# Kernel optimization log

Measured on AMD Instinct MI355X. Metric: run time of the kernel, lower is better.

Reference implementation:

```python
import jax, jax.numpy as jnp
import numpy as np

B, S, QD = 4, 2048, 1024
NH, KVH, DH = 16, 4, 64
WIN = 256  # sliding_window


def setup_inputs() -> dict:
    key = jax.random.key(0)
    ks = jax.random.split(key, 5)
    s = QD ** -0.5
    return {
        "hidden_states": jax.random.normal(ks[0], (B, S, QD), jnp.float32),
        "Wq": jax.random.normal(ks[1], (QD, NH * DH), jnp.float32) * s,
        "Wk": jax.random.normal(ks[2], (QD, KVH * DH), jnp.float32) * s,
        "Wv": jax.random.normal(ks[3], (QD, KVH * DH), jnp.float32) * s,
        "Wo": jax.random.normal(ks[4], (NH * DH, QD), jnp.float32) * s,
    }


def reference(hidden_states, Wq, Wk, Wv, Wo):
    x = hidden_states
    # QKV projections (torch Linear, no bias)
    q = (x @ Wq).reshape(B, S, NH, DH).transpose(0, 2, 1, 3)    # [B,NH,S,DH]
    k = (x @ Wk).reshape(B, S, KVH, DH).transpose(0, 2, 1, 3)   # [B,KVH,S,DH]
    v = (x @ Wv).reshape(B, S, KVH, DH).transpose(0, 2, 1, 3)
    # GQA: instead of repeat_interleave on k/v, group query heads per kv head
    g = NH // KVH
    qg = q.reshape(B, KVH, g, S, DH)
    scale = DH ** -0.5
    scores = jnp.einsum('bkgsd,bktd->bkgst', qg, k) * scale      # [B,KVH,g,S,S]
    # Sliding-window mask: torch SDPA treats a FLOAT mask as ADDITIVE, and the
    # original builds a 0/1 float mask (1 where |i-j| <= window). Faithful: add it.
    idx = jnp.arange(S)
    win = (jnp.abs(idx[:, None] - idx[None, :]) <= WIN).astype(scores.dtype)  # [S,S]
    scores = scores + win  # broadcast over B,KVH,g (same mask for all batch/heads)
    attn = jax.nn.softmax(scores, axis=-1)
    out = jnp.einsum('bkgst,bktd->bkgsd', attn, v)               # [B,KVH,g,S,DH]
    out = out.reshape(B, NH, S, DH).transpose(0, 2, 1, 3).reshape(B, S, NH * DH)
    return out @ Wo
```

## Files before the change

### kernel.cpp

```cpp
#include <hip/hip_runtime.h>
#include <hip/hip_bf16.h>


using short8 = __attribute__((ext_vector_type(8))) short;
using f32x4  = __attribute__((ext_vector_type(4))) float;
using f32x16 = __attribute__((ext_vector_type(16))) float;
using uint2v = __attribute__((ext_vector_type(2))) unsigned int;

#define GLDS(g, l) __builtin_amdgcn_global_load_lds( \
    (const __attribute__((address_space(1))) void*)(g), \
    (__attribute__((address_space(3))) void*)(l), 16, 0, 0)

__device__ __forceinline__ unsigned short f2bf(float f) {
  union { float f; unsigned u; } v; v.f = f;
  unsigned r = v.u + 0x7fffu + ((v.u >> 16) & 1u);
  return (unsigned short)(r >> 16);
}

__device__ __forceinline__ unsigned cvtpk(float lo, float hi) {
  unsigned r;
  asm("v_cvt_pk_bf16_f32 %0, %1, %2" : "=v"(r) : "v"(lo), "v"(hi));
  return r;
}

__global__ void cvt_x_kernel(const float* __restrict__ X, unsigned short* __restrict__ Xb) {
  int i = (blockIdx.x * blockDim.x + threadIdx.x) * 4;
  float4 v = *reinterpret_cast<const float4*>(X + i);
  ushort4 o;
  o.x = f2bf(v.x); o.y = f2bf(v.y); o.z = f2bf(v.z); o.w = f2bf(v.w);
  *reinterpret_cast<ushort4*>(Xb + i) = o;
}

__global__ __launch_bounds__(256) void wtr_kernel(
    const float* __restrict__ Wq, const float* __restrict__ Wk,
    const float* __restrict__ Wv, const float* __restrict__ Wo,
    unsigned short* __restrict__ WqkvT, unsigned short* __restrict__ WoT)
{
  __shared__ float tile[32][33];
  const int bx = blockIdx.x;
  const int by = blockIdx.y;
  const float* src; unsigned short* dst; int C, ct;
  if (by < 32)      { src = Wq; dst = WqkvT;               C = 1024; ct = by; }
  else if (by < 40) { src = Wk; dst = WqkvT + 1024 * 1024; C = 256;  ct = by - 32; }
  else if (by < 48) { src = Wv; dst = WqkvT + 1280 * 1024; C = 256;  ct = by - 40; }
  else              { src = Wo; dst = WoT;                 C = 1024; ct = by - 48; }
  const int tx = threadIdx.x & 31, ty = threadIdx.x >> 5;
  const int c0 = ct * 32, r0 = bx * 32;
#pragma unroll
  for (int i = 0; i < 4; ++i)
    tile[ty + i * 8][tx] = src[(size_t)(r0 + ty + i * 8) * C + c0 + tx];
  __syncthreads();
#pragma unroll
  for (int i = 0; i < 4; ++i) {
    int c = ty + i * 8;
    dst[(size_t)(c0 + c) * 1024 + r0 + tx] = f2bf(tile[tx][c]);
  }
}

template<int MODE>
__global__ __launch_bounds__(256) void gemm_bt_kernel(
    const unsigned short* __restrict__ A, const unsigned short* __restrict__ Bt,
    unsigned short* __restrict__ Qo, unsigned short* __restrict__ Ko,
    unsigned short* __restrict__ Vto, float* __restrict__ Co)
{
  __shared__ __align__(16) unsigned short As[128 * 32];
  __shared__ __align__(16) unsigned short Bs[128 * 32];
  const int m0 = blockIdx.x * 128;
  const int n0 = (MODE == 2 ? 1280 : 0) + blockIdx.y * 128;
  const int t = threadIdx.x;
  const int w = t >> 6, l = t & 63;
  const int wr = w >> 1, wc = w & 1;

  f32x4 acc[4][4] = {};

  const size_t aoff = (size_t)(m0 + w * 16 + (l >> 2)) * 1024 + (size_t)((l & 3) * 8);
  const size_t boff = (size_t)(n0 + w * 16 + (l >> 2)) * 1024 + (size_t)((l & 3) * 8);

  for (int kt = 0; kt < 1024; kt += 32) {
    GLDS(A  + aoff + kt,             &As[w * 512]);
    GLDS(A  + aoff + 64 * 1024 + kt, &As[(w + 4) * 512]);
    GLDS(Bt + boff + kt,             &Bs[w * 512]);
    GLDS(Bt + boff + 64 * 1024 + kt, &Bs[(w + 4) * 512]);
    __syncthreads();

    short8 af[4], bfr[4];
#pragma unroll
    for (int mi = 0; mi < 4; ++mi) {
      int row = wr * 64 + mi * 16 + (l & 15);
      af[mi] = *reinterpret_cast<const short8*>(&As[row * 32 + (l >> 4) * 8]);
    }
#pragma unroll
    for (int ni = 0; ni < 4; ++ni) {
      int row = wc * 64 + ni * 16 + (l & 15);
      bfr[ni] = *reinterpret_cast<const short8*>(&Bs[row * 32 + (l >> 4) * 8]);
    }
#pragma unroll
    for (int mi = 0; mi < 4; ++mi)
#pragma unroll
      for (int ni = 0; ni < 4; ++ni) {
        if (MODE == 0)
          acc[mi][ni] = __builtin_amdgcn_mfma_f32_16x16x32_bf16(bfr[ni], af[mi], acc[mi][ni], 0, 0, 0);
        else
          acc[mi][ni] = __builtin_amdgcn_mfma_f32_16x16x32_bf16(af[mi], bfr[ni], acc[mi][ni], 0, 0, 0);
      }
    __syncthreads();
  }

  const int lo = (l >> 4) * 4;

  if (MODE == 0) {
#pragma unroll
    for (int mi = 0; mi < 4; ++mi) {
      const int tok = m0 + wr * 64 + mi * 16 + (l & 15);
      const int bb = tok >> 11, ss = tok & 2047;
      const size_t bT = (size_t)bb * 16, T5 = ss >> 5, q5 = ss & 31;
#pragma unroll
      for (int ni = 0; ni < 4; ++ni) {
        const int ddb = n0 + wc * 64 + ni * 16;
        uint2 wv;
        wv.x = cvtpk(acc[mi][ni][0], acc[mi][ni][1]);
        wv.y = cvtpk(acc[mi][ni][2], acc[mi][ni][3]);
        size_t base; unsigned short* dstp;
        if (ddb < 1024) {
          int hh = ddb >> 6, kk = (ddb >> 4) & 3;
          base = ((((size_t)(bb * 16 + hh)) * 64 + T5) * 4 + kk) * 512; dstp = Qo;
        } else {
          int kvh = (ddb - 1024) >> 6, kk = (ddb >> 4) & 3;
          base = ((((size_t)(bb * 4 + kvh)) * 64 + T5) * 4 + kk) * 512; dstp = Ko;
        }
        *reinterpret_cast<uint2*>(dstp + base + (lo >> 3) * 256 + q5 * 8 + (lo & 7)) = wv;
      }
    }
  } else if (MODE == 2) {
#pragma unroll
    for (int ni = 0; ni < 4; ++ni) {
      const int dd = n0 + wc * 64 + ni * 16 + (l & 15);
      const int kvh = (dd - 1280) >> 6, d6 = dd & 63;
#pragma unroll
      for (int mi = 0; mi < 4; ++mi) {
        const int tokb = m0 + wr * 64 + mi * 16 + lo;
        const int bb = tokb >> 11, ss = tokb & 2047;
        const int T5 = ss >> 5;
        const int f = (d6 >> 5) * 2 + (mi & 1);
        uint2 wv;
        wv.x = cvtpk(acc[mi][ni][0], acc[mi][ni][1]);
        wv.y = cvtpk(acc[mi][ni][2], acc[mi][ni][3]);
        size_t base = ((((size_t)(bb * 4 + kvh)) * 64 + T5) * 4 + f) * 512;
        *reinterpret_cast<uint2*>(Vto + base + ((lo >> 3) & 1) * 256 + (d6 & 31) * 8 + (lo & 7)) = wv;
      }
    }
  } else {
#pragma unroll
    for (int mi = 0; mi < 4; ++mi)
#pragma unroll
      for (int ni = 0; ni < 4; ++ni)
#pragma unroll
        for (int r = 0; r < 4; ++r) {
          int m = m0 + wr * 64 + mi * 16 + lo + r;
          int n = n0 + wc * 64 + ni * 16 + (l & 15);
          Co[((size_t)m << 10) + n] = acc[mi][ni][r];
        }
  }
}

__global__ __launch_bounds__(256, 4) void attn_kernel(
    const unsigned short* __restrict__ Qf, const unsigned short* __restrict__ Kf,
    const unsigned short* __restrict__ Vf, unsigned short* __restrict__ AO)
{
  const int t = threadIdx.x, w = t >> 6, l = t & 63;
  const int hi = l >> 5, ln = l & 31;

  const int orig = blockIdx.x;
  const int swz = (orig & 7) * 128 + (orig >> 3);
  const int hf = swz >> 4;
  const int qt = swz & 15;
  const int b = hf >> 4, h = hf & 15, kvh = h >> 2;
  const int q0 = qt * 128 + w * 32;
  const int qrow = q0 + ln;

  const unsigned short* Qp = Qf + (((size_t)hf * 64 + qt * 4 + w) * 4) * 512;
  const unsigned short* Kt = Kf + ((size_t)(b * 4 + kvh) * 256) * 512 + l * 8;
  const unsigned short* Vt = Vf + ((size_t)(b * 4 + kvh) * 256) * 512 + l * 8;

  short8 qf[4];
#pragma unroll
  for (int kk = 0; kk < 4; ++kk)
    qf[kk] = *reinterpret_cast<const short8*>(Qp + kk * 512 + l * 8);

  f32x16 oA = {}, oB = {};
  float lsum = 0.f;
  const float C1  = 0.125f * 1.44269504f;
  const float L2E = 1.44269504f;
  const float FM  = 12.0f;

  for (int T = 0; T < 64; ++T) {
    short8 kf0 = *reinterpret_cast<const short8*>(Kt);
    short8 kf1 = *reinterpret_cast<const short8*>(Kt + 512);
    short8 kf2 = *reinterpret_cast<const short8*>(Kt + 1024);
    short8 kf3 = *reinterpret_cast<const short8*>(Kt + 1536);
    f32x16 s = {};
    s = __builtin_amdgcn_mfma_f32_32x32x16_bf16(kf0, qf[0], s, 0, 0, 0);
    s = __builtin_amdgcn_mfma_f32_32x32x16_bf16(kf1, qf[1], s, 0, 0, 0);
    s = __builtin_amdgcn_mfma_f32_32x32x16_bf16(kf2, qf[2], s, 0, 0, 0);
    s = __builtin_amdgcn_mfma_f32_32x32x16_bf16(kf3, qf[3], s, 0, 0, 0);
    short8 vf0 = *reinterpret_cast<const short8*>(Vt);
    short8 vf1 = *reinterpret_cast<const short8*>(Vt + 512);
    short8 vf2 = *reinterpret_cast<const short8*>(Vt + 1024);
    short8 vf3 = *reinterpret_cast<const short8*>(Vt + 1536);
    Kt += 2048; Vt += 2048;

    const int kv0 = T * 32;
    const int d = q0 - kv0;
    float p[16];
    if (d == 256 || d == -256) {
      const int qmb = qrow - kv0 - 4 * hi;
#pragma unroll
      for (int r = 0; r < 16; ++r) {
        const int kc = (r & 3) + 8 * (r >> 2);
        int df = qmb - kc; df = df < 0 ? -df : df;
        p[r] = __builtin_amdgcn_exp2f(
            __builtin_fmaf(s[r], C1, (df <= 256 ? L2E : 0.f) - FM));
      }
    } else {
      const float cc = ((d <= 224 && d >= -224) ? L2E : 0.f) - FM;
#pragma unroll
      for (int i = 0; i < 16; ++i)
        p[i] = __builtin_amdgcn_exp2f(__builtin_fmaf(s[i], C1, cc));
    }

    float s8[8], s4[4];
#pragma unroll
    for (int i = 0; i < 8; ++i) s8[i] = p[i] + p[i + 8];
#pragma unroll
    for (int i = 0; i < 4; ++i) s4[i] = s8[i] + s8[i + 4];
    float sum = (s4[0] + s4[1]) + (s4[2] + s4[3]);
    {
      uint2v sw = __builtin_amdgcn_permlane32_swap(__float_as_uint(sum), __float_as_uint(sum), false, false);
      sum = __uint_as_float(sw[0]) + __uint_as_float(sw[1]);
    }
    lsum += sum;

#pragma unroll
    for (int ks = 0; ks < 2; ++ks) {
      unsigned a0 = cvtpk(p[ks * 8 + 0], p[ks * 8 + 1]);
      unsigned a1 = cvtpk(p[ks * 8 + 2], p[ks * 8 + 3]);
      unsigned b0 = cvtpk(p[ks * 8 + 4], p[ks * 8 + 5]);
      unsigned b1 = cvtpk(p[ks * 8 + 6], p[ks * 8 + 7]);
      uint2v s0 = __builtin_amdgcn_permlane32_swap(a0, b0, false, false);
      uint2v s1 = __builtin_amdgcn_permlane32_swap(a1, b1, false, false);
      union { unsigned u[4]; short8 v; } pf;
      pf.u[0] = s0[0]; pf.u[1] = s1[0]; pf.u[2] = s0[1]; pf.u[3] = s1[1];
      oA = __builtin_amdgcn_mfma_f32_32x32x16_bf16(ks ? vf1 : vf0, pf.v, oA, 0, 0, 0);
      oB = __builtin_amdgcn_mfma_f32_32x32x16_bf16(ks ? vf3 : vf2, pf.v, oB, 0, 0, 0);
    }
  }

  const float inv = 1.f / lsum;
  unsigned short* Op = AO + ((size_t)(b * 2048 + qrow)) * 1024 + h * 64;
#pragma unroll
  for (int qd = 0; qd < 4; ++qd) {
    uint2 wv;
    wv.x = cvtpk(oA[4 * qd + 0] * inv, oA[4 * qd + 1] * inv);
    wv.y = cvtpk(oA[4 * qd + 2] * inv, oA[4 * qd + 3] * inv);
    *reinterpret_cast<uint2*>(Op + qd * 8 + hi * 4) = wv;
  }
#pragma unroll
  for (int qd = 0; qd < 4; ++qd) {
    uint2 wv;
    wv.x = cvtpk(oB[4 * qd + 0] * inv, oB[4 * qd + 1] * inv);
    wv.y = cvtpk(oB[4 * qd + 2] * inv, oB[4 * qd + 3] * inv);
    *reinterpret_cast<uint2*>(Op + 32 + qd * 8 + hi * 4) = wv;
  }
}

extern "C" void kernel_launch(void* const* d_in, const int* in_sizes, int n_in,
                              void* d_out, int out_size, void* d_ws, size_t ws_size,
                              hipStream_t stream)
{
  const float* X  = (const float*)d_in[0];
  const float* Wq = (const float*)d_in[1];
  const float* Wk = (const float*)d_in[2];
  const float* Wv = (const float*)d_in[3];
  const float* Wo = (const float*)d_in[4];
  float* out = (float*)d_out;
  char* ws = (char*)d_ws;

  unsigned short* Xb    = (unsigned short*)(ws);
  unsigned short* WqkvT = (unsigned short*)(ws + 16777216);
  unsigned short* WoT   = (unsigned short*)(ws + 19922944);
  unsigned short* Q     = (unsigned short*)(ws + 22020096);
  unsigned short* Kc    = (unsigned short*)(ws + 38797312);
  unsigned short* Vt    = (unsigned short*)(ws + 42991616);
  unsigned short* AO    = (unsigned short*)(ws + 47185920);

  cvt_x_kernel<<<8192, 256, 0, stream>>>(X, Xb);
  wtr_kernel<<<dim3(32, 80), 256, 0, stream>>>(Wq, Wk, Wv, Wo, WqkvT, WoT);

  gemm_bt_kernel<0><<<dim3(64, 10), 256, 0, stream>>>(Xb, WqkvT, Q, Kc, nullptr, nullptr);
  gemm_bt_kernel<2><<<dim3(64, 2),  256, 0, stream>>>(Xb, WqkvT, nullptr, nullptr, Vt, nullptr);
  attn_kernel<<<1024, 256, 0, stream>>>(Q, Kc, Vt, AO);
  gemm_bt_kernel<1><<<dim3(64, 8),  256, 0, stream>>>(AO, WoT, nullptr, nullptr, nullptr, out);
}
```

Before: 200.8 us.

## Fuse fp32-to-bf16 conversion of X into QKV GEMM and merge Q/K/V launches

Drops the standalone kernel that converts X to bf16. The QKV GEMM now reads fp32 X directly, converts it in registers with v_cvt_pk_bf16_f32, and writes the bf16 tile to LDS. The separate QK and V GEMM launches are merged into one 64x12 grid that chooses operand order and epilogue from n0. This removes a full bf16 round trip of X through memory and one launch. In exchange, each QKV block re-reads fp32 X, twice the bytes of bf16, across 12 column tiles, and loses the async global_load_lds path for the A operand.

```diff
diff --git a/kernel.cpp b/kernel.cpp
--- a/kernel.cpp
+++ b/kernel.cpp
@@ -21,14 +21,6 @@
   unsigned r;
   asm("v_cvt_pk_bf16_f32 %0, %1, %2" : "=v"(r) : "v"(lo), "v"(hi));
   return r;
-}
-
-__global__ void cvt_x_kernel(const float* __restrict__ X, unsigned short* __restrict__ Xb) {
-  int i = (blockIdx.x * blockDim.x + threadIdx.x) * 4;
-  float4 v = *reinterpret_cast<const float4*>(X + i);
-  ushort4 o;
-  o.x = f2bf(v.x); o.y = f2bf(v.y); o.z = f2bf(v.z); o.w = f2bf(v.w);
-  *reinterpret_cast<ushort4*>(Xb + i) = o;
 }
 
 __global__ __launch_bounds__(256) void wtr_kernel(
@@ -57,16 +49,15 @@
   }
 }
 
-template<int MODE>
-__global__ __launch_bounds__(256) void gemm_bt_kernel(
-    const unsigned short* __restrict__ A, const unsigned short* __restrict__ Bt,
+__global__ __launch_bounds__(256) void qkv_gemm_kernel(
+    const float* __restrict__ X, const unsigned short* __restrict__ Bt,
     unsigned short* __restrict__ Qo, unsigned short* __restrict__ Ko,
-    unsigned short* __restrict__ Vto, float* __restrict__ Co)
+    unsigned short* __restrict__ Vto)
 {
   __shared__ __align__(16) unsigned short As[128 * 32];
   __shared__ __align__(16) unsigned short Bs[128 * 32];
   const int m0 = blockIdx.x * 128;
-  const int n0 = (MODE == 2 ? 1280 : 0) + blockIdx.y * 128;
+  const int n0 = blockIdx.y * 128;
   const int t = threadIdx.x;
   const int w = t >> 6, l = t & 63;
   const int wr = w >> 1, wc = w & 1;
@@ -75,12 +66,24 @@
 
   const size_t aoff = (size_t)(m0 + w * 16 + (l >> 2)) * 1024 + (size_t)((l & 3) * 8);
   const size_t boff = (size_t)(n0 + w * 16 + (l >> 2)) * 1024 + (size_t)((l & 3) * 8);
+  unsigned short* Aw0 = &As[w * 512 + l * 8];
+  unsigned short* Aw1 = &As[(w + 4) * 512 + l * 8];
+  const bool qk = (n0 < 1280);
 
   for (int kt = 0; kt < 1024; kt += 32) {
-    GLDS(A  + aoff + kt,             &As[w * 512]);
-    GLDS(A  + aoff + 64 * 1024 + kt, &As[(w + 4) * 512]);
     GLDS(Bt + boff + kt,             &Bs[w * 512]);
     GLDS(Bt + boff + 64 * 1024 + kt, &Bs[(w + 4) * 512]);
+    float4 fa0 = *reinterpret_cast<const float4*>(X + aoff + kt);
+    float4 fa1 = *reinterpret_cast<const float4*>(X + aoff + kt + 4);
+    float4 fb0 = *reinterpret_cast<const float4*>(X + aoff + 64 * 1024 + kt);
+    float4 fb1 = *reinterpret_cast<const float4*>(X + aoff + 64 * 1024 + kt + 4);
+    uint4 ua, ub;
+    ua.x = cvtpk(fa0.x, fa0.y); ua.y = cvtpk(fa0.z, fa0.w);
+    ua.z = cvtpk(fa1.x, fa1.y); ua.w = cvtpk(fa1.z, fa1.w);
+    ub.x = cvtpk(fb0.x, fb0.y); ub.y = cvtpk(fb0.z, fb0.w);
+    ub.z = cvtpk(fb1.x, fb1.y); ub.w = cvtpk(fb1.z, fb1.w);
+    *reinterpret_cast<uint4*>(Aw0) = ua;
+    *reinterpret_cast<uint4*>(Aw1) = ub;
     __syncthreads();
 
     short8 af[4], bfr[4];
@@ -94,26 +97,30 @@
       int row = wc * 64 + ni * 16 + (l & 15);
       bfr[ni] = *reinterpret_cast<const short8*>(&Bs[row * 32 + (l >> 4) * 8]);
     }
-#pragma unroll
-    for (int mi = 0; mi < 4; ++mi)
-#pragma unroll
-      for (int ni = 0; ni < 4; ++ni) {
-        if (MODE == 0)
+    if (qk) {
+#pragma unroll
+      for (int mi = 0; mi < 4; ++mi)
+#pragma unroll
+        for (int ni = 0; ni < 4; ++ni)
           acc[mi][ni] = __builtin_amdgcn_mfma_f32_16x16x32_bf16(bfr[ni], af[mi], acc[mi][ni], 0, 0, 0);
-        else
+    } else {
+#pragma unroll
+      for (int mi = 0; mi < 4; ++mi)
+#pragma unroll
+        for (int ni = 0; ni < 4; ++ni)
           acc[mi][ni] = __builtin_amdgcn_mfma_f32_16x16x32_bf16(af[mi], bfr[ni], acc[mi][ni], 0, 0, 0);
-      }
+    }
     __syncthreads();
   }
 
   const int lo = (l >> 4) * 4;
 
-  if (MODE == 0) {
+  if (qk) {
 #pragma unroll
     for (int mi = 0; mi < 4; ++mi) {
       const int tok = m0 + wr * 64 + mi * 16 + (l & 15);
       const int bb = tok >> 11, ss = tok & 2047;
-      const size_t bT = (size_t)bb * 16, T5 = ss >> 5, q5 = ss & 31;
+      const int T5 = ss >> 5, q5 = ss & 31;
 #pragma unroll
       for (int ni = 0; ni < 4; ++ni) {
         const int ddb = n0 + wc * 64 + ni * 16;
@@ -131,7 +138,7 @@
         *reinterpret_cast<uint2*>(dstp + base + (lo >> 3) * 256 + q5 * 8 + (lo & 7)) = wv;
       }
     }
-  } else if (MODE == 2) {
+  } else {
 #pragma unroll
     for (int ni = 0; ni < 4; ++ni) {
       const int dd = n0 + wc * 64 + ni * 16 + (l & 15);
@@ -149,18 +156,62 @@
         *reinterpret_cast<uint2*>(Vto + base + ((lo >> 3) & 1) * 256 + (d6 & 31) * 8 + (lo & 7)) = wv;
       }
     }
-  } else {
+  }
+}
+
+__global__ __launch_bounds__(256) void outproj_gemm_kernel(
+    const unsigned short* __restrict__ A, const unsigned short* __restrict__ Bt,
+    float* __restrict__ Co)
+{
+  __shared__ __align__(16) unsigned short As[128 * 32];
+  __shared__ __align__(16) unsigned short Bs[128 * 32];
+  const int m0 = blockIdx.x * 128;
+  const int n0 = blockIdx.y * 128;
+  const int t = threadIdx.x;
+  const int w = t >> 6, l = t & 63;
+  const int wr = w >> 1, wc = w & 1;
+
+  f32x4 acc[4][4] = {};
+
+  const size_t aoff = (size_t)(m0 + w * 16 + (l >> 2)) * 1024 + (size_t)((l & 3) * 8);
+  const size_t boff = (size_t)(n0 + w * 16 + (l >> 2)) * 1024 + (size_t)((l & 3) * 8);
+
+  for (int kt = 0; kt < 1024; kt += 32) {
+    GLDS(A  + aoff + kt,             &As[w * 512]);
+    GLDS(A  + aoff + 64 * 1024 + kt, &As[(w + 4) * 512]);
+    GLDS(Bt + boff + kt,             &Bs[w * 512]);
+    GLDS(Bt + boff + 64 * 1024 + kt, &Bs[(w + 4) * 512]);
+    __syncthreads();
+
+    short8 af[4], bfr[4];
+#pragma unroll
+    for (int mi = 0; mi < 4; ++mi) {
+      int row = wr * 64 + mi * 16 + (l & 15);
+      af[mi] = *reinterpret_cast<const short8*>(&As[row * 32 + (l >> 4) * 8]);
+    }
+#pragma unroll
+    for (int ni = 0; ni < 4; ++ni) {
+      int row = wc * 64 + ni * 16 + (l & 15);
+      bfr[ni] = *reinterpret_cast<const short8*>(&Bs[row * 32 + (l >> 4) * 8]);
+    }
 #pragma unroll
     for (int mi = 0; mi < 4; ++mi)
 #pragma unroll
       for (int ni = 0; ni < 4; ++ni)
-#pragma unroll
-        for (int r = 0; r < 4; ++r) {
-          int m = m0 + wr * 64 + mi * 16 + lo + r;
-          int n = n0 + wc * 64 + ni * 16 + (l & 15);
-          Co[((size_t)m << 10) + n] = acc[mi][ni][r];
-        }
-  }
+        acc[mi][ni] = __builtin_amdgcn_mfma_f32_16x16x32_bf16(af[mi], bfr[ni], acc[mi][ni], 0, 0, 0);
+    __syncthreads();
+  }
+
+#pragma unroll
+  for (int mi = 0; mi < 4; ++mi)
+#pragma unroll
+    for (int ni = 0; ni < 4; ++ni)
+#pragma unroll
+      for (int r = 0; r < 4; ++r) {
+        int m = m0 + wr * 64 + mi * 16 + (l >> 4) * 4 + r;
+        int n = n0 + wc * 64 + ni * 16 + (l & 15);
+        Co[((size_t)m << 10) + n] = acc[mi][ni][r];
+      }
 }
 
 __global__ __launch_bounds__(256, 4) void attn_kernel(
@@ -285,19 +336,15 @@
   float* out = (float*)d_out;
   char* ws = (char*)d_ws;
 
-  unsigned short* Xb    = (unsigned short*)(ws);
-  unsigned short* WqkvT = (unsigned short*)(ws + 16777216);
-  unsigned short* WoT   = (unsigned short*)(ws + 19922944);
-  unsigned short* Q     = (unsigned short*)(ws + 22020096);
-  unsigned short* Kc    = (unsigned short*)(ws + 38797312);
-  unsigned short* Vt    = (unsigned short*)(ws + 42991616);
-  unsigned short* AO    = (unsigned short*)(ws + 47185920);
-
-  cvt_x_kernel<<<8192, 256, 0, stream>>>(X, Xb);
+  unsigned short* WqkvT = (unsigned short*)(ws);
+  unsigned short* WoT   = (unsigned short*)(ws + 3145728);
+  unsigned short* Q     = (unsigned short*)(ws + 5242880);
+  unsigned short* Kc    = (unsigned short*)(ws + 22020096);
+  unsigned short* Vt    = (unsigned short*)(ws + 26214400);
+  unsigned short* AO    = (unsigned short*)(ws + 30408704);
+
   wtr_kernel<<<dim3(32, 80), 256, 0, stream>>>(Wq, Wk, Wv, Wo, WqkvT, WoT);
-
-  gemm_bt_kernel<0><<<dim3(64, 10), 256, 0, stream>>>(Xb, WqkvT, Q, Kc, nullptr, nullptr);
-  gemm_bt_kernel<2><<<dim3(64, 2),  256, 0, stream>>>(Xb, WqkvT, nullptr, nullptr, Vt, nullptr);
+  qkv_gemm_kernel<<<dim3(64, 12), 256, 0, stream>>>(X, WqkvT, Q, Kc, Vt);
   attn_kernel<<<1024, 256, 0, stream>>>(Q, Kc, Vt, AO);
-  gemm_bt_kernel<1><<<dim3(64, 8),  256, 0, stream>>>(AO, WoT, nullptr, nullptr, nullptr, out);
-}
+  outproj_gemm_kernel<<<dim3(64, 8), 256, 0, stream>>>(AO, WoT, out);
+}
```

New measurement: 198.5 us. Within noise of the previous version (-1.1%).
